# Optimization experiments

Measured on AMD Instinct MI355X. Metric: run time of the kernel, lower is better.

The kernel has to match this reference:

```python
import jax, jax.numpy as jnp
import numpy as np


def setup_inputs() -> dict:
    key = jax.random.key(0)
    ks = jax.random.split(key, 6)
    B, T, D, U = 32, 2048, 512, 512
    scale = 1.0 / np.sqrt(D)
    return {
        "values": jax.random.normal(ks[0], (B, T, D), dtype=jnp.float32),
        "query": jax.random.normal(ks[1], (B, D), dtype=jnp.float32),
        "W1": jax.random.normal(ks[2], (D, U), dtype=jnp.float32) * scale,
        "b1": jnp.zeros((U,), dtype=jnp.float32),
        "W2": jax.random.normal(ks[3], (D, U), dtype=jnp.float32) * scale,
        "b2": jnp.zeros((U,), dtype=jnp.float32),
        "V": jax.random.normal(ks[4], (U, 1), dtype=jnp.float32) * (1.0 / np.sqrt(U)),
        "bV": jnp.zeros((1,), dtype=jnp.float32),
    }


def reference(values, query, W1, b1, W2, b2, V, bV):
    # values: [B,T,D], query: [B,D]
    proj_v = jnp.einsum("btd,du->btu", values, W1) + b1          # [B,T,U]
    proj_q = (query @ W2 + b2)[:, None, :]                        # [B,1,U]
    score = jnp.tanh(proj_v + proj_q) @ V + bV                    # [B,T,1]
    attention_weights = jax.nn.softmax(score, axis=1)             # [B,T,1]
    context_vector = jnp.sum(attention_weights * values, axis=1)  # [B,D]
    return context_vector, attention_weights
```

## Files before the change

kernel.cpp:

```cpp
#include <hip/hip_runtime.h>
#include <math.h>


#define B_ 32
#define T_ 2048
#define D_ 512
#define U_ 512
#define M_ (B_ * T_)

typedef _Float16 half8 __attribute__((ext_vector_type(8)));
typedef _Float16 half4 __attribute__((ext_vector_type(4)));
typedef float floatx4 __attribute__((ext_vector_type(4)));

__device__ __forceinline__ float fast_tanh(float x) {
  x = fminf(fmaxf(x, -20.f), 20.f);
  const float e = __expf(2.f * x);
  return 1.f - 2.f / (e + 1.f);
}

__device__ __forceinline__ void load_lds16(const _Float16* g, _Float16* l) {
  __builtin_amdgcn_global_load_lds(
      (const __attribute__((address_space(1))) void*)g,
      (__attribute__((address_space(3))) void*)l, 16, 0, 0);
}

__global__ __launch_bounds__(256) void prep_fused(
    const float* __restrict__ values, const float* __restrict__ W1,
    const float* __restrict__ query, const float* __restrict__ W2,
    const float* __restrict__ b2, _Float16* __restrict__ valf16,
    _Float16* __restrict__ w1t, float* __restrict__ projq,
    float* __restrict__ scores, float* __restrict__ context, int do_cvt) {
  __shared__ float sh[64 * 65];
  const int bx = blockIdx.x;
  const int tid = threadIdx.x;
  if (bx < 8192) {
    if (!do_cvt) return;
    const long base = (long)bx * 4096;
#pragma unroll
    for (int j = 0; j < 4; ++j) {
      const long idx = base + j * 1024 + tid * 4;
      const float4 a = *(const float4*)(values + idx);
      half4 h = {(_Float16)a.x, (_Float16)a.y, (_Float16)a.z, (_Float16)a.w};
      *(half4*)(valf16 + idx) = h;
    }
  } else if (bx < 8256) {
    const int t = bx - 8192;
    const int k0 = (t >> 3) * 64, u0 = (t & 7) * 64;
    float(*sm)[65] = (float(*)[65])sh;
    const int lu = tid & 63;
    const int g = tid >> 6;
#pragma unroll
    for (int i = 0; i < 16; ++i) {
      const int row = g * 16 + i;
      sm[row][lu] = W1[(long)(k0 + row) * U_ + u0 + lu];
    }
    __syncthreads();
#pragma unroll
    for (int i = 0; i < 16; ++i) {
      const int row = g * 16 + i;
      w1t[(long)(u0 + row) * D_ + k0 + lu] = (_Float16)sm[lu][row];
    }
  } else {
    const int t = bx - 8256;
    const int gid = t * 256 + tid;
    context[gid] = 0.f;
    ((float4*)scores)[gid] = make_float4(0.f, 0.f, 0.f, 0.f);
    const int b = t >> 1;
    const int u = (t & 1) * 256 + tid;
    for (int d = tid; d < D_; d += 256) sh[d] = query[b * D_ + d];
    __syncthreads();
    float acc = 0.f;
#pragma unroll 8
    for (int d = 0; d < D_; ++d) acc += sh[d] * W2[d * U_ + u];
    projq[b * U_ + u] = acc + b2[u];
  }
}

__global__ __launch_bounds__(256, 2) void score_dma_kernel(
    const _Float16* __restrict__ valf16, const _Float16* __restrict__ w1t,
    const float* __restrict__ b1, const float* __restrict__ projq,
    const float* __restrict__ V, float* __restrict__ scores) {
  const int m0 = blockIdx.x * 256;
  const int b = blockIdx.x >> 3;
  const int u0 = blockIdx.y * 128;
  const int tid = threadIdx.x;
  const int lane = tid & 63;
  const int w = tid >> 6;
  const int wm = (w & 1) * 128;
  const int wn = u0 + (w >> 1) * 64;
  const int ln = lane & 15;
  const int lq = lane >> 4;

  __shared__ alignas(16) _Float16 As[256 * 32];
  __shared__ float red[2][256];

  const int rl = lane >> 2;
  const int cg = (lane & 3) ^ (rl & 3);
  const _Float16* gA[4];
  _Float16* lA[4];
#pragma unroll
  for (int j = 0; j < 4; ++j) {
    const int r = w * 64 + j * 16 + rl;
    gA[j] = valf16 + (long)(m0 + r) * D_ + cg * 8;
    lA[j] = &As[(w * 64 + j * 16) * 32];
  }

  const _Float16* bp[4];
#pragma unroll
  for (int ni = 0; ni < 4; ++ni)
    bp[ni] = w1t + (long)(wn + ni * 16 + ln) * D_ + lq * 8;

  const int aswz = (lq ^ (ln & 3)) * 8;

  floatx4 acc[8][4] = {};

  for (int k0 = 0; k0 < D_; k0 += 32) {
#pragma unroll
    for (int j = 0; j < 4; ++j) load_lds16(gA[j] + k0, lA[j]);
    half8 bf[4];
#pragma unroll
    for (int ni = 0; ni < 4; ++ni) bf[ni] = *(const half8*)(bp[ni] + k0);
    __syncthreads();
    half8 af[8];
#pragma unroll
    for (int mi = 0; mi < 8; ++mi)
      af[mi] = *(const half8*)&As[(wm + mi * 16 + ln) * 32 + aswz];
#pragma unroll
    for (int mi = 0; mi < 8; ++mi)
#pragma unroll
      for (int ni = 0; ni < 4; ++ni)
        acc[mi][ni] = __builtin_amdgcn_mfma_f32_16x16x32_f16(
            af[mi], bf[ni], acc[mi][ni], 0, 0, 0);
    __syncthreads();
  }

  float pre[4], vv[4];
#pragma unroll
  for (int ni = 0; ni < 4; ++ni) {
    const int u = wn + ni * 16 + ln;
    pre[ni] = b1[u] + projq[b * U_ + u];
    vv[ni] = V[u];
  }
#pragma unroll
  for (int mi = 0; mi < 8; ++mi) {
#pragma unroll
    for (int r = 0; r < 4; ++r) {
      float t = 0.f;
#pragma unroll
      for (int ni = 0; ni < 4; ++ni)
        t += fast_tanh(acc[mi][ni][r] + pre[ni]) * vv[ni];
      t += __shfl_xor(t, 1);
      t += __shfl_xor(t, 2);
      t += __shfl_xor(t, 4);
      t += __shfl_xor(t, 8);
      if (ln == 0) red[w >> 1][wm + mi * 16 + lq * 4 + r] = t;
    }
  }
  __syncthreads();
  atomicAdd(scores + m0 + tid, red[0][tid] + red[1][tid]);
}

__global__ __launch_bounds__(256) void score_lds_kernel(
    const float* __restrict__ values, const _Float16* __restrict__ w1t,
    const float* __restrict__ b1, const float* __restrict__ projq,
    const float* __restrict__ V, float* __restrict__ scores) {
  const int m0 = blockIdx.x * 128;
  const int u0 = blockIdx.y * 128;
  const int b = blockIdx.x >> 4;
  const int tid = threadIdx.x;
  const int lane = tid & 63;
  const int w = tid >> 6;
  const int wm = (w & 1) * 64;
  const int wn = (w >> 1) * 64;
  const int ln = lane & 15;
  const int lq = lane >> 4;
  __shared__ alignas(16) _Float16 As[128 * 40];
  const int srow = tid >> 1;
  const int skoff = (tid & 1) * 16;
  const float* aptr = values + (long)(m0 + srow) * D_ + skoff;
  _Float16* awr = &As[srow * 40 + skoff];
  const _Float16* bBase = w1t + (long)(u0 + wn + ln) * D_ + lq * 8;
  floatx4 acc[4][4] = {};
  for (int k0 = 0; k0 < D_; k0 += 32) {
    const float4 a0 = *(const float4*)(aptr + k0);
    const float4 a1 = *(const float4*)(aptr + k0 + 4);
    const float4 a2 = *(const float4*)(aptr + k0 + 8);
    const float4 a3 = *(const float4*)(aptr + k0 + 12);
    half8 bf[4];
#pragma unroll
    for (int ni = 0; ni < 4; ++ni)
      bf[ni] = *(const half8*)(bBase + (long)ni * 16 * D_ + k0);
    half8 h0 = {(_Float16)a0.x, (_Float16)a0.y, (_Float16)a0.z, (_Float16)a0.w,
                (_Float16)a1.x, (_Float16)a1.y, (_Float16)a1.z, (_Float16)a1.w};
    half8 h1 = {(_Float16)a2.x, (_Float16)a2.y, (_Float16)a2.z, (_Float16)a2.w,
                (_Float16)a3.x, (_Float16)a3.y, (_Float16)a3.z, (_Float16)a3.w};
    *(half8*)awr = h0;
    *(half8*)(awr + 8) = h1;
    __syncthreads();
    half8 af[4];
#pragma unroll
    for (int i = 0; i < 4; ++i)
      af[i] = *(const half8*)&As[(wm + i * 16 + ln) * 40 + lq * 8];
#pragma unroll
    for (int mi = 0; mi < 4; ++mi)
#pragma unroll
      for (int ni = 0; ni < 4; ++ni)
        acc[mi][ni] = __builtin_amdgcn_mfma_f32_16x16x32_f16(
            af[mi], bf[ni], acc[mi][ni], 0, 0, 0);
    __syncthreads();
  }
  float pre[4], vv[4];
#pragma unroll
  for (int ni = 0; ni < 4; ++ni) {
    const int u = u0 + wn + ni * 16 + ln;
    pre[ni] = b1[u] + projq[b * U_ + u];
    vv[ni] = V[u];
  }
#pragma unroll
  for (int mi = 0; mi < 4; ++mi) {
#pragma unroll
    for (int r = 0; r < 4; ++r) {
      float t = 0.f;
#pragma unroll
      for (int ni = 0; ni < 4; ++ni)
        t += fast_tanh(acc[mi][ni][r] + pre[ni]) * vv[ni];
      t += __shfl_xor(t, 1);
      t += __shfl_xor(t, 2);
      t += __shfl_xor(t, 4);
      t += __shfl_xor(t, 8);
      if (ln == mi * 4 + r)
        atomicAdd(scores + m0 + wm + mi * 16 + lq * 4 + r, t);
    }
  }
}

__global__ __launch_bounds__(256) void softmax_context_kernel(
    const float* __restrict__ scores, const float* __restrict__ values,
    float* __restrict__ weights, float* __restrict__ context) {
  const int b = blockIdx.x;
  const int t0 = blockIdx.y * 64;
  const int tid = threadIdx.x;

  float v[8];
  float mx = -INFINITY;
#pragma unroll
  for (int i = 0; i < 8; ++i) {
    v[i] = scores[b * T_ + i * 256 + tid];
    mx = fmaxf(mx, v[i]);
  }
#pragma unroll
  for (int off = 32; off > 0; off >>= 1) mx = fmaxf(mx, __shfl_down(mx, off));
  __shared__ float sm[4], ss[4];
  if ((tid & 63) == 0) sm[tid >> 6] = mx;
  __syncthreads();
  mx = fmaxf(fmaxf(sm[0], sm[1]), fmaxf(sm[2], sm[3]));
  float sum = 0.f;
#pragma unroll
  for (int i = 0; i < 8; ++i) sum += __expf(v[i] - mx);
#pragma unroll
  for (int off = 32; off > 0; off >>= 1) sum += __shfl_down(sum, off);
  if ((tid & 63) == 0) ss[tid >> 6] = sum;
  __syncthreads();
  const float inv = 1.f / (ss[0] + ss[1] + ss[2] + ss[3]);

  __shared__ float wsh[64];
  if (tid < 64) {
    const float ww = __expf(scores[b * T_ + t0 + tid] - mx) * inv;
    wsh[tid] = ww;
    weights[b * T_ + t0 + tid] = ww;
  }
  __syncthreads();

  const int g = tid >> 7;
  const int dx = tid & 127;
  __shared__ float4 part[128];
  float4 acc = make_float4(0.f, 0.f, 0.f, 0.f);
  const float4* vp = (const float4*)(values + (long)(b * T_ + t0 + g) * D_) + dx;
#pragma unroll 4
  for (int t = 0; t < 32; ++t) {
    const float4 x = vp[(long)(2 * t) * (D_ / 4)];
    const float ww = wsh[2 * t + g];
    acc.x += ww * x.x; acc.y += ww * x.y; acc.z += ww * x.z; acc.w += ww * x.w;
  }
  if (g == 0) part[dx] = acc;
  __syncthreads();
  if (g == 1) {
    const float4 p = part[dx];
    atomicAdd(&context[b * D_ + dx * 4 + 0], acc.x + p.x);
    atomicAdd(&context[b * D_ + dx * 4 + 1], acc.y + p.y);
    atomicAdd(&context[b * D_ + dx * 4 + 2], acc.z + p.z);
    atomicAdd(&context[b * D_ + dx * 4 + 3], acc.w + p.w);
  }
}

extern "C" void kernel_launch(void* const* d_in, const int* in_sizes, int n_in,
                              void* d_out, int out_size, void* d_ws, size_t ws_size,
                              hipStream_t stream) {
  const float* values = (const float*)d_in[0];
  const float* query = (const float*)d_in[1];
  const float* W1 = (const float*)d_in[2];
  const float* b1 = (const float*)d_in[3];
  const float* W2 = (const float*)d_in[4];
  const float* b2 = (const float*)d_in[5];
  const float* V = (const float*)d_in[6];

  float* out = (float*)d_out;
  float* context = out;
  float* weights = out + B_ * D_;
  float* projq = (float*)d_ws;
  float* scores = projq + B_ * U_;
  _Float16* w1t = (_Float16*)((char*)d_ws + 65536 + 262144);
  _Float16* valf16 = (_Float16*)((char*)d_ws + 851968);

  const int dma = ws_size >= (size_t)851968 + (size_t)M_ * D_ * 2;

  prep_fused<<<8320, 256, 0, stream>>>(values, W1, query, W2, b2, valf16, w1t,
                                       projq, scores, context, dma);
  if (dma) {
    score_dma_kernel<<<dim3(M_ / 256, U_ / 128), 256, 0, stream>>>(
        valf16, w1t, b1, projq, V, scores);
  } else {
    score_lds_kernel<<<dim3(M_ / 128, U_ / 128), 256, 0, stream>>>(
        values, w1t, b1, projq, V, scores);
  }
  softmax_context_kernel<<<dim3(B_, T_ / 64), 256, 0, stream>>>(
      scores, values, weights, context);
}
```

Measured before the change: 335.2 us.

## Fuse fp32-to-fp16 conversion into score GEMM with full-U tiles and double buffering

Drops the separate pass that converts values to fp16 in workspace. The score kernel now DMA-loads fp32 values straight into double-buffered LDS and converts them to fp16 while building MFMA fragments. Each 512-thread block covers all 512 U columns for 128 rows, so scores are written directly instead of being zeroed and accumulated with atomics. This removes a full write and reread of the fp16 copy of values (64 MB), at the cost of more LDS traffic per tile, in-loop conversion work, and one block per CU with larger register use.

```diff
diff --git a/kernel.cpp b/kernel.cpp
--- a/kernel.cpp
+++ b/kernel.cpp
@@ -9,7 +9,6 @@
 #define M_ (B_ * T_)
 
 typedef _Float16 half8 __attribute__((ext_vector_type(8)));
-typedef _Float16 half4 __attribute__((ext_vector_type(4)));
 typedef float floatx4 __attribute__((ext_vector_type(4)));
 
 __device__ __forceinline__ float fast_tanh(float x) {
@@ -18,33 +17,22 @@
   return 1.f - 2.f / (e + 1.f);
 }
 
-__device__ __forceinline__ void load_lds16(const _Float16* g, _Float16* l) {
+__device__ __forceinline__ void load_lds16f(const float* g, float* l) {
   __builtin_amdgcn_global_load_lds(
       (const __attribute__((address_space(1))) void*)g,
       (__attribute__((address_space(3))) void*)l, 16, 0, 0);
 }
 
 __global__ __launch_bounds__(256) void prep_fused(
-    const float* __restrict__ values, const float* __restrict__ W1,
-    const float* __restrict__ query, const float* __restrict__ W2,
-    const float* __restrict__ b2, _Float16* __restrict__ valf16,
+    const float* __restrict__ W1, const float* __restrict__ query,
+    const float* __restrict__ W2, const float* __restrict__ b2,
     _Float16* __restrict__ w1t, float* __restrict__ projq,
-    float* __restrict__ scores, float* __restrict__ context, int do_cvt) {
+    float* __restrict__ context) {
   __shared__ float sh[64 * 65];
   const int bx = blockIdx.x;
   const int tid = threadIdx.x;
-  if (bx < 8192) {
-    if (!do_cvt) return;
-    const long base = (long)bx * 4096;
-#pragma unroll
-    for (int j = 0; j < 4; ++j) {
-      const long idx = base + j * 1024 + tid * 4;
-      const float4 a = *(const float4*)(values + idx);
-      half4 h = {(_Float16)a.x, (_Float16)a.y, (_Float16)a.z, (_Float16)a.w};
-      *(half4*)(valf16 + idx) = h;
-    }
-  } else if (bx < 8256) {
-    const int t = bx - 8192;
+  if (bx < 64) {
+    const int t = bx;
     const int k0 = (t >> 3) * 64, u0 = (t & 7) * 64;
     float(*sm)[65] = (float(*)[65])sh;
     const int lu = tid & 63;
@@ -61,10 +49,9 @@
       w1t[(long)(u0 + row) * D_ + k0 + lu] = (_Float16)sm[lu][row];
     }
   } else {
-    const int t = bx - 8256;
+    const int t = bx - 64;
     const int gid = t * 256 + tid;
     context[gid] = 0.f;
-    ((float4*)scores)[gid] = make_float4(0.f, 0.f, 0.f, 0.f);
     const int b = t >> 1;
     const int u = (t & 1) * 256 + tid;
     for (int d = tid; d < D_; d += 256) sh[d] = query[b * D_ + d];
@@ -76,78 +63,89 @@
   }
 }
 
-__global__ __launch_bounds__(256, 2) void score_dma_kernel(
-    const _Float16* __restrict__ valf16, const _Float16* __restrict__ w1t,
+__global__ __launch_bounds__(512, 1) void score_fused(
+    const float* __restrict__ values, const _Float16* __restrict__ w1t,
     const float* __restrict__ b1, const float* __restrict__ projq,
     const float* __restrict__ V, float* __restrict__ scores) {
-  const int m0 = blockIdx.x * 256;
-  const int b = blockIdx.x >> 3;
-  const int u0 = blockIdx.y * 128;
+  const int m0 = blockIdx.x * 128;
+  const int b = blockIdx.x >> 4;
   const int tid = threadIdx.x;
   const int lane = tid & 63;
   const int w = tid >> 6;
-  const int wm = (w & 1) * 128;
-  const int wn = u0 + (w >> 1) * 64;
+  const int wm = (w & 1) * 64;
+  const int wu = (w >> 1) * 128;
   const int ln = lane & 15;
   const int lq = lane >> 4;
 
-  __shared__ alignas(16) _Float16 As[256 * 32];
-  __shared__ float red[2][256];
-
-  const int rl = lane >> 2;
-  const int cg = (lane & 3) ^ (rl & 3);
-  const _Float16* gA[4];
-  _Float16* lA[4];
-#pragma unroll
-  for (int j = 0; j < 4; ++j) {
-    const int r = w * 64 + j * 16 + rl;
-    gA[j] = valf16 + (long)(m0 + r) * D_ + cg * 8;
-    lA[j] = &As[(w * 64 + j * 16) * 32];
-  }
-
-  const _Float16* bp[4];
-#pragma unroll
-  for (int ni = 0; ni < 4; ++ni)
-    bp[ni] = w1t + (long)(wn + ni * 16 + ln) * D_ + lq * 8;
-
-  const int aswz = (lq ^ (ln & 3)) * 8;
-
-  floatx4 acc[8][4] = {};
-
-  for (int k0 = 0; k0 < D_; k0 += 32) {
-#pragma unroll
-    for (int j = 0; j < 4; ++j) load_lds16(gA[j] + k0, lA[j]);
-    half8 bf[4];
-#pragma unroll
-    for (int ni = 0; ni < 4; ++ni) bf[ni] = *(const half8*)(bp[ni] + k0);
-    __syncthreads();
-    half8 af[8];
-#pragma unroll
-    for (int mi = 0; mi < 8; ++mi)
-      af[mi] = *(const half8*)&As[(wm + mi * 16 + ln) * 32 + aswz];
-#pragma unroll
-    for (int mi = 0; mi < 8; ++mi)
-#pragma unroll
-      for (int ni = 0; ni < 4; ++ni)
+  __shared__ alignas(16) float As[2][128 * 32];
+  __shared__ float red[4][128];
+
+  const int dr = lane >> 3;
+  const int dc = (lane & 7) ^ dr;
+  const float* gA[2];
+#pragma unroll
+  for (int j = 0; j < 2; ++j) {
+    const int r = w * 16 + j * 8 + dr;
+    gA[j] = values + (long)(m0 + r) * D_ + dc * 4;
+  }
+
+  const _Float16* bp[8];
+#pragma unroll
+  for (int ni = 0; ni < 8; ++ni)
+    bp[ni] = w1t + (long)(wu + ni * 16 + ln) * D_ + lq * 8;
+
+  floatx4 acc[4][8] = {};
+
+#pragma unroll
+  for (int j = 0; j < 2; ++j)
+    load_lds16f(gA[j], &As[0][(w * 16 + j * 8) * 32]);
+  __syncthreads();
+
+  for (int t = 0; t < 16; ++t) {
+    const int p = t & 1;
+    half8 bf[8];
+#pragma unroll
+    for (int ni = 0; ni < 8; ++ni) bf[ni] = *(const half8*)(bp[ni] + t * 32);
+    if (t < 15) {
+#pragma unroll
+      for (int j = 0; j < 2; ++j)
+        load_lds16f(gA[j] + (t + 1) * 32,
+                    &As[p ^ 1][(w * 16 + j * 8) * 32]);
+    }
+    half8 af[4];
+#pragma unroll
+    for (int mi = 0; mi < 4; ++mi) {
+      const int r = wm + mi * 16 + ln;
+      const float* row = &As[p][r * 32];
+      const float4 lo = *(const float4*)(row + (((2 * lq) ^ (r & 7)) * 4));
+      const float4 hi = *(const float4*)(row + (((2 * lq + 1) ^ (r & 7)) * 4));
+      af[mi] = half8{(_Float16)lo.x, (_Float16)lo.y, (_Float16)lo.z,
+                     (_Float16)lo.w, (_Float16)hi.x, (_Float16)hi.y,
+                     (_Float16)hi.z, (_Float16)hi.w};
+    }
+#pragma unroll
+    for (int mi = 0; mi < 4; ++mi)
+#pragma unroll
+      for (int ni = 0; ni < 8; ++ni)
         acc[mi][ni] = __builtin_amdgcn_mfma_f32_16x16x32_f16(
             af[mi], bf[ni], acc[mi][ni], 0, 0, 0);
     __syncthreads();
   }
 
-  float pre[4], vv[4];
-#pragma unroll
-  for (int ni = 0; ni < 4; ++ni) {
-    const int u = wn + ni * 16 + ln;
+  float pre[8], vv[8];
+#pragma unroll
+  for (int ni = 0; ni < 8; ++ni) {
+    const int u = wu + ni * 16 + ln;
     pre[ni] = b1[u] + projq[b * U_ + u];
     vv[ni] = V[u];
   }
 #pragma unroll
-  for (int mi = 0; mi < 8; ++mi) {
+  for (int mi = 0; mi < 4; ++mi) {
 #pragma unroll
     for (int r = 0; r < 4; ++r) {
       float t = 0.f;
 #pragma unroll
-      for (int ni = 0; ni < 4; ++ni)
+      for (int ni = 0; ni < 8; ++ni)
         t += fast_tanh(acc[mi][ni][r] + pre[ni]) * vv[ni];
       t += __shfl_xor(t, 1);
       t += __shfl_xor(t, 2);
@@ -157,81 +155,9 @@
     }
   }
   __syncthreads();
-  atomicAdd(scores + m0 + tid, red[0][tid] + red[1][tid]);
-}
-
-__global__ __launch_bounds__(256) void score_lds_kernel(
-    const float* __restrict__ values, const _Float16* __restrict__ w1t,
-    const float* __restrict__ b1, const float* __restrict__ projq,
-    const float* __restrict__ V, float* __restrict__ scores) {
-  const int m0 = blockIdx.x * 128;
-  const int u0 = blockIdx.y * 128;
-  const int b = blockIdx.x >> 4;
-  const int tid = threadIdx.x;
-  const int lane = tid & 63;
-  const int w = tid >> 6;
-  const int wm = (w & 1) * 64;
-  const int wn = (w >> 1) * 64;
-  const int ln = lane & 15;
-  const int lq = lane >> 4;
-  __shared__ alignas(16) _Float16 As[128 * 40];
-  const int srow = tid >> 1;
-  const int skoff = (tid & 1) * 16;
-  const float* aptr = values + (long)(m0 + srow) * D_ + skoff;
-  _Float16* awr = &As[srow * 40 + skoff];
-  const _Float16* bBase = w1t + (long)(u0 + wn + ln) * D_ + lq * 8;
-  floatx4 acc[4][4] = {};
-  for (int k0 = 0; k0 < D_; k0 += 32) {
-    const float4 a0 = *(const float4*)(aptr + k0);
-    const float4 a1 = *(const float4*)(aptr + k0 + 4);
-    const float4 a2 = *(const float4*)(aptr + k0 + 8);
-    const float4 a3 = *(const float4*)(aptr + k0 + 12);
-    half8 bf[4];
-#pragma unroll
-    for (int ni = 0; ni < 4; ++ni)
-      bf[ni] = *(const half8*)(bBase + (long)ni * 16 * D_ + k0);
-    half8 h0 = {(_Float16)a0.x, (_Float16)a0.y, (_Float16)a0.z, (_Float16)a0.w,
-                (_Float16)a1.x, (_Float16)a1.y, (_Float16)a1.z, (_Float16)a1.w};
-    half8 h1 = {(_Float16)a2.x, (_Float16)a2.y, (_Float16)a2.z, (_Float16)a2.w,
-                (_Float16)a3.x, (_Float16)a3.y, (_Float16)a3.z, (_Float16)a3.w};
-    *(half8*)awr = h0;
-    *(half8*)(awr + 8) = h1;
-    __syncthreads();
-    half8 af[4];
-#pragma unroll
-    for (int i = 0; i < 4; ++i)
-      af[i] = *(const half8*)&As[(wm + i * 16 + ln) * 40 + lq * 8];
-#pragma unroll
-    for (int mi = 0; mi < 4; ++mi)
-#pragma unroll
-      for (int ni = 0; ni < 4; ++ni)
-        acc[mi][ni] = __builtin_amdgcn_mfma_f32_16x16x32_f16(
-            af[mi], bf[ni], acc[mi][ni], 0, 0, 0);
-    __syncthreads();
-  }
-  float pre[4], vv[4];
-#pragma unroll
-  for (int ni = 0; ni < 4; ++ni) {
-    const int u = u0 + wn + ni * 16 + ln;
-    pre[ni] = b1[u] + projq[b * U_ + u];
-    vv[ni] = V[u];
-  }
-#pragma unroll
-  for (int mi = 0; mi < 4; ++mi) {
-#pragma unroll
-    for (int r = 0; r < 4; ++r) {
-      float t = 0.f;
-#pragma unroll
-      for (int ni = 0; ni < 4; ++ni)
-        t += fast_tanh(acc[mi][ni][r] + pre[ni]) * vv[ni];
-      t += __shfl_xor(t, 1);
-      t += __shfl_xor(t, 2);
-      t += __shfl_xor(t, 4);
-      t += __shfl_xor(t, 8);
-      if (ln == mi * 4 + r)
-        atomicAdd(scores + m0 + wm + mi * 16 + lq * 4 + r, t);
-    }
-  }
+  if (tid < 128)
+    scores[m0 + tid] =
+        red[0][tid] + red[1][tid] + red[2][tid] + red[3][tid];
 }
 
 __global__ __launch_bounds__(256) void softmax_context_kernel(
@@ -310,19 +236,9 @@
   float* projq = (float*)d_ws;
   float* scores = projq + B_ * U_;
   _Float16* w1t = (_Float16*)((char*)d_ws + 65536 + 262144);
-  _Float16* valf16 = (_Float16*)((char*)d_ws + 851968);
-
-  const int dma = ws_size >= (size_t)851968 + (size_t)M_ * D_ * 2;
-
-  prep_fused<<<8320, 256, 0, stream>>>(values, W1, query, W2, b2, valf16, w1t,
-                                       projq, scores, context, dma);
-  if (dma) {
-    score_dma_kernel<<<dim3(M_ / 256, U_ / 128), 256, 0, stream>>>(
-        valf16, w1t, b1, projq, V, scores);
-  } else {
-    score_lds_kernel<<<dim3(M_ / 128, U_ / 128), 256, 0, stream>>>(
-        values, w1t, b1, projq, V, scores);
-  }
+
+  prep_fused<<<128, 256, 0, stream>>>(W1, query, W2, b2, w1t, projq, context);
+  score_fused<<<M_ / 128, 512, 0, stream>>>(values, w1t, b1, projq, V, scores);
   softmax_context_kernel<<<dim3(B_, T_ / 64), 256, 0, stream>>>(
       scores, values, weights, context);
 }
```

After: 318.9 us. 4.9% less time.
